# Kernel optimization log

Hardware: AMD Instinct MI355X
Metric: run time of the kernel (lower is better)

The kernel has to match this reference:

```python
import jax, jax.numpy as jnp
import numpy as np

D_MODEL = 1024
HEADS = 16
D_K = D_MODEL // HEADS
B, S = 2, 2048


def setup_inputs() -> dict:
    key = jax.random.key(0)
    ks = jax.random.split(key, 11)
    sc = 1.0 / np.sqrt(D_MODEL)
    return {
        "q": jax.random.normal(ks[0], (B, S, D_MODEL), jnp.float32),
        "k": jax.random.normal(ks[1], (B, S, D_MODEL), jnp.float32),
        "v": jax.random.normal(ks[2], (B, S, D_MODEL), jnp.float32),
        "Wq": jax.random.normal(ks[3], (D_MODEL, D_MODEL), jnp.float32) * sc,
        "bq": jnp.zeros((D_MODEL,), jnp.float32),
        "Wk": jax.random.normal(ks[4], (D_MODEL, D_MODEL), jnp.float32) * sc,
        "bk": jnp.zeros((D_MODEL,), jnp.float32),
        "Wv": jax.random.normal(ks[5], (D_MODEL, D_MODEL), jnp.float32) * sc,
        "bv": jnp.zeros((D_MODEL,), jnp.float32),
        "Wo": jax.random.normal(ks[6], (D_MODEL, D_MODEL), jnp.float32) * sc,
        "bo": jnp.zeros((D_MODEL,), jnp.float32),
    }


def reference(q, k, v, Wq, bq, Wk, bk, Wv, bv, Wo, bo):
    bs = q.shape[0]
    # linear projections then split heads: [B,S,D] -> [B,H,S,Dk]
    def proj(x, W, b):
        y = x @ W.T + b
        return y.reshape(bs, -1, HEADS, D_K).transpose(0, 2, 1, 3)

    qh = proj(q, Wq, bq)
    kh = proj(k, Wk, bk)
    vh = proj(v, Wv, bv)
    # scores: [B,H,Sq,Sk] -- full attention matrix as in the original
    scores = jnp.einsum("bhqd,bhkd->bhqk", qh, kh) / jnp.sqrt(
        jnp.asarray(D_K, jnp.float32))
    attn = jax.nn.softmax(scores, axis=-1)
    # dropout is identity in eval/reference mode
    out = jnp.einsum("bhqk,bhkd->bhqd", attn, vh)
    concat = out.transpose(0, 2, 1, 3).reshape(bs, -1, D_MODEL)
    return concat @ Wo.T + bo
```

## Files before the change

kernel.cpp:

```cpp
#include <hip/hip_runtime.h>
#include <hip/hip_bf16.h>

typedef __attribute__((ext_vector_type(8))) short bf16x8;
typedef __attribute__((ext_vector_type(4))) float f32x4;
typedef __attribute__((ext_vector_type(16))) float f32x16;

#define DM   1024
#define SEQ  2048
#define NB   2
#define NH   16
#define MR   (NB*SEQ)

#define SMK  (MR*DM)
#define W1M  (DM*DM)

#define QSCALE 0.18033688011112042f

#define OFF_QB  ((size_t)0)
#define OFF_WO  ((size_t)(3*(size_t)SMK + 3*(size_t)W1M))
#define OFF_QP  ((size_t)(3*(size_t)SMK + 4*(size_t)W1M))
#define OFF_KP  ((size_t)(4*(size_t)SMK + 4*(size_t)W1M))
#define OFF_VP  ((size_t)(5*(size_t)SMK + 4*(size_t)W1M))
#define OFF_CC  ((size_t)0)

__device__ __forceinline__ unsigned short f2bf(float f) {
  union { __hip_bfloat16 b; unsigned short u; } cv;
  cv.b = __float2bfloat16(f);
  return cv.u;
}

__device__ __forceinline__ unsigned int cvtpk_bf16(float lo, float hi) {
  unsigned int r;
  asm("v_cvt_pk_bf16_f32 %0, %1, %2" : "=v"(r) : "v"(lo), "v"(hi));
  return r;
}

__device__ __forceinline__ void plane32_swap(unsigned int& a, unsigned int& b) {
  asm("v_permlane32_swap_b32 %0, %1" : "+v"(a), "+v"(b));
}

__global__ __launch_bounds__(256) void cvt_wo(const float* __restrict__ wo,
                                              unsigned short* __restrict__ dst) {
  int i = blockIdx.x * 256 + threadIdx.x;
  float4 v = reinterpret_cast<const float4*>(wo)[i];
  ushort4 o;
  o.x = f2bf(v.x); o.y = f2bf(v.y); o.z = f2bf(v.z); o.w = f2bf(v.w);
  reinterpret_cast<ushort4*>(dst)[i] = o;
}

__device__ __forceinline__ void gload_lds16(const void* g, void* l) {
  __builtin_amdgcn_global_load_lds(
      (const __attribute__((address_space(1))) unsigned int*)g,
      (__attribute__((address_space(3))) unsigned int*)l,
      16, 0, 0);
}

template<bool BIAS_ROW>
__device__ __forceinline__ void gemm_f32_body(unsigned short* __restrict__ As,
                                              unsigned short* __restrict__ Bs,
                                              const float* __restrict__ A,
                                              const float* __restrict__ B,
                                              const float* __restrict__ bias,
                                              unsigned short* __restrict__ C,
                                              int N, int K, float scale,
                                              int brow, int bcol) {
  const int tid  = threadIdx.x;
  const int lane = tid & 63;
  const int w    = tid >> 6;
  const int wr   = w >> 1, wc = w & 1;

  f32x4 acc[4][4];
#pragma unroll
  for (int m = 0; m < 4; m++)
#pragma unroll
    for (int n = 0; n < 4; n++) acc[m][n] = (f32x4){0.f, 0.f, 0.f, 0.f};

  const int srow = lane >> 2;
  const int scol = (lane & 3) * 8;

  f32x4 fa[2][2], fb[2][2];

  auto loadst = [&](int k0) {
#pragma unroll
    for (int i = 0; i < 2; i++) {
      const float* pa = A + (size_t)(brow + (w + i * 4) * 16 + srow) * K + k0 + scol;
      fa[i][0] = *(const f32x4*)pa;
      fa[i][1] = *(const f32x4*)(pa + 4);
      const float* pb = B + (size_t)(bcol + (w + i * 4) * 16 + srow) * K + k0 + scol;
      fb[i][0] = *(const f32x4*)pb;
      fb[i][1] = *(const f32x4*)(pb + 4);
    }
  };
  auto commit = [&](int buf) {
#pragma unroll
    for (int i = 0; i < 2; i++) {
      union { unsigned int u[4]; bf16x8 v8; } ua, ub;
#pragma unroll
      for (int j = 0; j < 2; j++) {
        ua.u[2 * j]     = cvtpk_bf16(fa[i][j][0], fa[i][j][1]);
        ua.u[2 * j + 1] = cvtpk_bf16(fa[i][j][2], fa[i][j][3]);
        ub.u[2 * j]     = cvtpk_bf16(fb[i][j][0], fb[i][j][1]);
        ub.u[2 * j + 1] = cvtpk_bf16(fb[i][j][2], fb[i][j][3]);
      }
      *(bf16x8*)((char*)As + (size_t)buf * 8192 + (w + i * 4) * 1024 + lane * 16) = ua.v8;
      *(bf16x8*)((char*)Bs + (size_t)buf * 8192 + (w + i * 4) * 1024 + lane * 16) = ub.v8;
    }
  };

  loadst(0);
  commit(0);
  loadst(32);

  const int nk = K / 32;
  const int lrow_a = wr * 64 + (lane & 15);
  const int lrow_b = wc * 64 + (lane & 15);
  const int lcol   = (lane >> 4) * 8;

  for (int kt = 0; kt < nk; ++kt) {
    int buf = kt & 1;
    asm volatile("s_waitcnt lgkmcnt(0)" ::: "memory");
    __builtin_amdgcn_s_barrier();
    __builtin_amdgcn_sched_barrier(0);
    if (kt + 1 < nk) commit(buf ^ 1);
    if (kt + 2 < nk) loadst((kt + 2) * 32);
    bf16x8 a[4], b[4];
#pragma unroll
    for (int m = 0; m < 4; m++)
      a[m] = *(const bf16x8*)&As[(size_t)buf * 4096 + (lrow_a + m * 16) * 32 + lcol];
#pragma unroll
    for (int n = 0; n < 4; n++)
      b[n] = *(const bf16x8*)&Bs[(size_t)buf * 4096 + (lrow_b + n * 16) * 32 + lcol];
    __builtin_amdgcn_s_setprio(1);
#pragma unroll
    for (int m = 0; m < 4; m++)
#pragma unroll
      for (int n = 0; n < 4; n++)
        acc[m][n] = __builtin_amdgcn_mfma_f32_16x16x32_bf16(a[m], b[n], acc[m][n], 0, 0, 0);
    __builtin_amdgcn_s_setprio(0);
  }

  const int crow0 = brow + wr * 64;
  const int ccol0 = bcol + wc * 64;
  const int rsub  = (lane >> 4) * 4;
  const int csub  = lane & 15;
#pragma unroll
  for (int m = 0; m < 4; m++)
#pragma unroll
    for (int n = 0; n < 4; n++) {
      int col = ccol0 + n * 16 + csub;
      float bcol_v = BIAS_ROW ? 0.f : bias[col];
#pragma unroll
      for (int qq = 0; qq < 4; qq++) {
        int row = crow0 + m * 16 + rsub + qq;
        float bb = BIAS_ROW ? bias[row] : bcol_v;
        C[(size_t)row * N + col] = f2bf((acc[m][n][qq] + bb) * scale);
      }
    }
}

__global__ __launch_bounds__(256, 3) void gemm_qkv(const float* __restrict__ q,
                                                   const float* __restrict__ k,
                                                   const float* __restrict__ v,
                                                   const float* __restrict__ Wq,
                                                   const float* __restrict__ Wk,
                                                   const float* __restrict__ Wv,
                                                   unsigned short* ws,
                                                   const float* __restrict__ bq,
                                                   const float* __restrict__ bk,
                                                   const float* __restrict__ bv) {
  __shared__ unsigned short As[2 * 128 * 32];
  __shared__ unsigned short Bs[2 * 128 * 32];
  const int i  = blockIdx.x;
  const int x  = i & 7;
  const int r  = i >> 3;
  const int pm = r >> 3;
  const int bx = r & 7;
  const int p  = x * 12 + pm;
  const int z  = p >> 5;
  const int by = p & 31;
  if (z < 2) {
    gemm_f32_body<false>(As, Bs,
                         z ? k : q, z ? Wk : Wq, z ? bk : bq,
                         ws + OFF_QP + (size_t)z * SMK,
                         DM, DM, z ? 1.f : QSCALE, by * 128, bx * 128);
  } else {
    gemm_f32_body<true>(As, Bs,
                        Wv, v, bv,
                        ws + OFF_VP,
                        MR, DM, 1.f, bx * 128, by * 128);
  }
}

__device__ __forceinline__ void gemm_out_body(unsigned short* __restrict__ As,
                                              unsigned short* __restrict__ Bs,
                                              const unsigned short* __restrict__ A,
                                              const unsigned short* __restrict__ Bt,
                                              const float* __restrict__ bias,
                                              float* __restrict__ Cv,
                                              int N, int K,
                                              int brow, int bcol) {
  constexpr int BM = 64, BN = 128;
  const int tid  = threadIdx.x;
  const int lane = tid & 63;
  const int w    = tid >> 6;
  const int wr   = w >> 1, wc = w & 1;

  f32x4 acc[2][4];
#pragma unroll
  for (int m = 0; m < 2; m++)
#pragma unroll
    for (int n = 0; n < 4; n++) acc[m][n] = (f32x4){0.f, 0.f, 0.f, 0.f};

  const int srow = lane >> 2;
  const int scol = (lane & 3) * 8;

  auto stage = [&](int buf, int k0) {
#pragma unroll
    for (int c = w; c < BM / 16; c += 4)
      gload_lds16(A + (size_t)(brow + c * 16 + srow) * K + k0 + scol,
                  (char*)As + (size_t)buf * BM * 64 + c * 1024);
#pragma unroll
    for (int c = w; c < BN / 16; c += 4)
      gload_lds16(Bt + (size_t)(bcol + c * 16 + srow) * K + k0 + scol,
                  (char*)Bs + (size_t)buf * BN * 64 + c * 1024);
  };

  stage(0, 0);
  stage(1, 32);

  const int nk = K / 32;
  const int lrow_a = wr * (BM / 2) + (lane & 15);
  const int lrow_b = wc * (BN / 2) + (lane & 15);
  const int lcol   = (lane >> 4) * 8;

  int b0 = 0;
  for (int kt = 0; kt < nk; ++kt) {
    if (kt + 1 < nk) asm volatile("s_waitcnt vmcnt(3)" ::: "memory");
    else             asm volatile("s_waitcnt vmcnt(0)" ::: "memory");
    __builtin_amdgcn_s_barrier();
    __builtin_amdgcn_sched_barrier(0);
    if (kt + 2 < nk) {
      int bn = b0 + 2; if (bn >= 3) bn -= 3;
      stage(bn, (kt + 2) * 32);
    }
    bf16x8 a[2], b[4];
#pragma unroll
    for (int m = 0; m < 2; m++)
      a[m] = *(const bf16x8*)&As[(size_t)b0 * BM * 32 + (lrow_a + m * 16) * 32 + lcol];
#pragma unroll
    for (int n = 0; n < 4; n++)
      b[n] = *(const bf16x8*)&Bs[(size_t)b0 * BN * 32 + (lrow_b + n * 16) * 32 + lcol];
    __builtin_amdgcn_s_setprio(1);
#pragma unroll
    for (int m = 0; m < 2; m++)
#pragma unroll
      for (int n = 0; n < 4; n++)
        acc[m][n] = __builtin_amdgcn_mfma_f32_16x16x32_bf16(a[m], b[n], acc[m][n], 0, 0, 0);
    __builtin_amdgcn_s_setprio(0);
    b0 = (b0 == 2) ? 0 : b0 + 1;
  }

  const int crow0 = brow + wr * (BM / 2);
  const int ccol0 = bcol + wc * (BN / 2);
  const int rsub  = (lane >> 4) * 4;
  const int csub  = lane & 15;
#pragma unroll
  for (int m = 0; m < 2; m++)
#pragma unroll
    for (int n = 0; n < 4; n++) {
      int col = ccol0 + n * 16 + csub;
      float bv = bias[col];
#pragma unroll
      for (int qq = 0; qq < 4; qq++) {
        int row = crow0 + m * 16 + rsub + qq;
        Cv[(size_t)row * N + col] = acc[m][n][qq] + bv;
      }
    }
}

__global__ __launch_bounds__(256) void gemm_out(const unsigned short* __restrict__ ws,
                                                const float* __restrict__ bo,
                                                float* __restrict__ out) {
  __shared__ unsigned short As[3 * 64 * 32];
  __shared__ unsigned short Bs[3 * 128 * 32];
  const int i  = blockIdx.x;
  const int x  = i & 7;
  const int r  = i >> 3;
  const int pm = r >> 3;
  const int bx = r & 7;
  const int by = x * 8 + pm;
  gemm_out_body(As, Bs,
                ws + OFF_CC, ws + OFF_WO, bo, out,
                DM, DM, by * 64, bx * 128);
}

__global__ __launch_bounds__(512, 4) void flash_attn(unsigned short* ws) {
  __shared__ __align__(16) unsigned char smem[65536];

  const int tid  = threadIdx.x;
  const int lane = tid & 63;
  const int w    = tid >> 6;
  const int s    = w >> 2;
  const int wsub = w & 3;
  const int q    = lane & 31;
  const int hi   = lane >> 5;
  const int swq  = q & 7;
  const int bid  = blockIdx.x;
  const int swzb = (bid & 7) * 64 + (bid >> 3);
  const int qblk = swzb & 15;
  const int bh   = swzb >> 4;
  const int b    = bh >> 4, h = bh & 15;

  const unsigned short* Qp = ws + OFF_QP;
  const unsigned short* Kp = ws + OFF_KP;
  const unsigned short* Vp = ws + OFF_VP;
  unsigned short* CC = ws + OFF_CC;

  const unsigned short* Kg = Kp + (size_t)(b * SEQ) * DM + h * 64;
  const unsigned short* Vg = Vp + (size_t)(h * 64) * MR + (size_t)b * SEQ;

  bf16x8 bqf[4];
  {
    const unsigned short* qrow =
        Qp + (size_t)(b * SEQ + qblk * 128 + wsub * 32 + q) * DM + h * 64;
#pragma unroll
    for (int c = 0; c < 4; c++)
      bqf[c] = *(const bf16x8*)(qrow + c * 16 + hi * 8);
  }

  f32x16 o_acc[2];
#pragma unroll
  for (int dt = 0; dt < 2; dt++)
#pragma unroll
    for (int r = 0; r < 16; r++) o_acc[dt][r] = 0.f;
  float l_run = 0.f;

  auto stage = [&](int buf, int t) {
    const unsigned short* Kt = Kg + (size_t)(s * 16 + t) * 64 * DM;
    const unsigned short* Vt = Vg + (s * 16 + t) * 64;
    char* base = (char*)smem + (size_t)(s * 2 + buf) * 16384;
#pragma unroll
    for (int i = 0; i < 2; i++) {
      int slot = wsub * 128 + i * 64 + lane;
      int srow = slot >> 3;
      int gch  = (slot & 7) ^ (srow & 7);
      gload_lds16(Kt + (size_t)srow * DM + gch * 8, base + slot * 16);
      gload_lds16(Vt + (size_t)srow * MR + gch * 8, base + 8192 + slot * 16);
    }
  };

  stage(0, 0);

  for (int t = 0; t < 16; ++t) {
    int buf = t & 1;
    __syncthreads();
    if (t + 1 < 16) stage(buf ^ 1, t + 1);
    const unsigned short* Kb = (const unsigned short*)(smem + (size_t)(s * 2 + buf) * 16384);
    const unsigned short* Vb = Kb + 4096;

    f32x16 st0, st1;
#pragma unroll
    for (int r = 0; r < 16; r++) { st0[r] = 0.f; st1[r] = 0.f; }
    __builtin_amdgcn_s_setprio(1);
#pragma unroll
    for (int c = 0; c < 4; c++) {
      int ch = (((c << 1) | hi) ^ swq) << 3;
      bf16x8 ak0 = *(const bf16x8*)&Kb[q * 64 + ch];
      bf16x8 ak1 = *(const bf16x8*)&Kb[(32 + q) * 64 + ch];
      st0 = __builtin_amdgcn_mfma_f32_32x32x16_bf16(ak0, bqf[c], st0, 0, 0, 0);
      st1 = __builtin_amdgcn_mfma_f32_32x32x16_bf16(ak1, bqf[c], st1, 0, 0, 0);
    }
    __builtin_amdgcn_s_setprio(0);

    unsigned int pk0[8], pk1[8];
    float lt = 0.f;
#pragma unroll
    for (int p = 0; p < 8; p++) {
      float a0 = __builtin_amdgcn_exp2f(st0[2 * p]);
      float a1 = __builtin_amdgcn_exp2f(st0[2 * p + 1]);
      float b0 = __builtin_amdgcn_exp2f(st1[2 * p]);
      float b1 = __builtin_amdgcn_exp2f(st1[2 * p + 1]);
      lt += (a0 + a1) + (b0 + b1);
      pk0[p] = cvtpk_bf16(a0, a1);
      pk1[p] = cvtpk_bf16(b0, b1);
    }
    l_run += lt;

    plane32_swap(pk0[0], pk0[2]); plane32_swap(pk0[1], pk0[3]);
    plane32_swap(pk0[4], pk0[6]); plane32_swap(pk0[5], pk0[7]);
    plane32_swap(pk1[0], pk1[2]); plane32_swap(pk1[1], pk1[3]);
    plane32_swap(pk1[4], pk1[6]); plane32_swap(pk1[5], pk1[7]);

    __builtin_amdgcn_s_setprio(1);
#pragma unroll
    for (int t4 = 0; t4 < 4; t4++) {
      union { unsigned int u[4]; bf16x8 v; } pb;
      const unsigned int* src = (t4 < 2) ? pk0 : pk1;
      pb.u[0] = src[(t4 & 1) * 4 + 0];
      pb.u[1] = src[(t4 & 1) * 4 + 1];
      pb.u[2] = src[(t4 & 1) * 4 + 2];
      pb.u[3] = src[(t4 & 1) * 4 + 3];
      int ch = (((t4 << 1) | hi) ^ swq) << 3;
#pragma unroll
      for (int dt = 0; dt < 2; dt++) {
        bf16x8 av = *(const bf16x8*)&Vb[(dt * 32 + q) * 64 + ch];
        o_acc[dt] = __builtin_amdgcn_mfma_f32_32x32x16_bf16(av, pb.v, o_acc[dt], 0, 0, 0);
      }
    }
    __builtin_amdgcn_s_setprio(0);
  }

  __syncthreads();
  float* scr = (float*)smem;
  float lsum = l_run + __shfl_xor(l_run, 32, 64);
  if (s == 1) {
    int idx = (wsub * 64 + lane) * 33;
#pragma unroll
    for (int dt = 0; dt < 2; dt++)
#pragma unroll
      for (int r = 0; r < 16; r++) scr[idx + dt * 16 + r] = o_acc[dt][r];
    scr[idx + 32] = lsum;
  }
  __syncthreads();
  if (s == 0) {
    int idx = (wsub * 64 + lane) * 33;
#pragma unroll
    for (int dt = 0; dt < 2; dt++)
#pragma unroll
      for (int r = 0; r < 16; r++) o_acc[dt][r] += scr[idx + dt * 16 + r];
    float l = lsum + scr[idx + 32];
    float inv = 1.f / l;

    int qg = b * SEQ + qblk * 128 + wsub * 32 + q;
    unsigned short* crow = CC + (size_t)qg * DM + h * 64;
#pragma unroll
    for (int dt = 0; dt < 2; dt++)
#pragma unroll
      for (int rq = 0; rq < 4; rq++) {
        ushort4 o;
        o.x = f2bf(o_acc[dt][4 * rq + 0] * inv);
        o.y = f2bf(o_acc[dt][4 * rq + 1] * inv);
        o.z = f2bf(o_acc[dt][4 * rq + 2] * inv);
        o.w = f2bf(o_acc[dt][4 * rq + 3] * inv);
        *(ushort4*)&crow[dt * 32 + rq * 8 + hi * 4] = o;
      }
  }
}

extern "C" void kernel_launch(void* const* d_in, const int* in_sizes, int n_in,
                              void* d_out, int out_size, void* d_ws, size_t ws_size,
                              hipStream_t stream) {
  const float* q  = (const float*)d_in[0];
  const float* k  = (const float*)d_in[1];
  const float* v  = (const float*)d_in[2];
  const float* Wq = (const float*)d_in[3];
  const float* bq = (const float*)d_in[4];
  const float* Wk = (const float*)d_in[5];
  const float* bk = (const float*)d_in[6];
  const float* Wv = (const float*)d_in[7];
  const float* bv = (const float*)d_in[8];
  const float* Wo = (const float*)d_in[9];
  const float* bo = (const float*)d_in[10];

  unsigned short* ws = (unsigned short*)d_ws;
  float* out = (float*)d_out;

  cvt_wo<<<dim3((W1M / 4) / 256), dim3(256), 0, stream>>>(Wo, ws + OFF_WO);

  gemm_qkv<<<dim3(768), dim3(256), 0, stream>>>(q, k, v, Wq, Wk, Wv, ws, bq, bk, bv);

  flash_attn<<<dim3(512), dim3(512), 0, stream>>>(ws);

  gemm_out<<<dim3(512), dim3(256), 0, stream>>>(ws, bo, out);
}
```

Measured before the change: 112.1 us.

## Deepen QKV GEMM pipeline to triple LDS buffers and two register stages

The fp32-input QKV projection GEMM moves from double to triple buffering in shared memory and keeps two register stages of global loads in flight, prefetching three k-tiles ahead. Fragment reads from LDS are now issued before the commit of the next tile, so the LDS write overlaps with the MFMA work. Launch bounds drop from 3 to 2 blocks per CU to allow for the extra registers and shared memory. The deeper prefetch is meant to hide global load latency, at the cost of lower occupancy.

```diff
diff --git a/kernel.cpp b/kernel.cpp
--- a/kernel.cpp
+++ b/kernel.cpp
@@ -78,9 +78,9 @@
   const int srow = lane >> 2;
   const int scol = (lane & 3) * 8;
 
-  f32x4 fa[2][2], fb[2][2];
-
-  auto loadst = [&](int k0) {
+  f32x4 fa0[2][2], fb0[2][2], fa1[2][2], fb1[2][2];
+
+  auto loadst = [&](int k0, f32x4 (&fa)[2][2], f32x4 (&fb)[2][2]) {
 #pragma unroll
     for (int i = 0; i < 2; i++) {
       const float* pa = A + (size_t)(brow + (w + i * 4) * 16 + srow) * K + k0 + scol;
@@ -91,7 +91,7 @@
       fb[i][1] = *(const f32x4*)(pb + 4);
     }
   };
-  auto commit = [&](int buf) {
+  auto commit = [&](int buf, f32x4 (&fa)[2][2], f32x4 (&fb)[2][2]) {
 #pragma unroll
     for (int i = 0; i < 2; i++) {
       union { unsigned int u[4]; bf16x8 v8; } ua, ub;
@@ -107,29 +107,32 @@
     }
   };
 
-  loadst(0);
-  commit(0);
-  loadst(32);
-
   const int nk = K / 32;
   const int lrow_a = wr * 64 + (lane & 15);
   const int lrow_b = wc * 64 + (lane & 15);
   const int lcol   = (lane >> 4) * 8;
 
-  for (int kt = 0; kt < nk; ++kt) {
-    int buf = kt & 1;
+  loadst(0, fa0, fb0);
+  commit(0, fa0, fb0);
+  loadst(32, fa1, fb1);
+  loadst(64, fa0, fb0);
+
+  int b_read = 0;
+
+  auto iter = [&](int kt, f32x4 (&fa)[2][2], f32x4 (&fb)[2][2]) {
     asm volatile("s_waitcnt lgkmcnt(0)" ::: "memory");
     __builtin_amdgcn_s_barrier();
     __builtin_amdgcn_sched_barrier(0);
-    if (kt + 1 < nk) commit(buf ^ 1);
-    if (kt + 2 < nk) loadst((kt + 2) * 32);
+    int b_write = b_read + 1; if (b_write == 3) b_write = 0;
     bf16x8 a[4], b[4];
 #pragma unroll
     for (int m = 0; m < 4; m++)
-      a[m] = *(const bf16x8*)&As[(size_t)buf * 4096 + (lrow_a + m * 16) * 32 + lcol];
+      a[m] = *(const bf16x8*)&As[(size_t)b_read * 4096 + (lrow_a + m * 16) * 32 + lcol];
 #pragma unroll
     for (int n = 0; n < 4; n++)
-      b[n] = *(const bf16x8*)&Bs[(size_t)buf * 4096 + (lrow_b + n * 16) * 32 + lcol];
+      b[n] = *(const bf16x8*)&Bs[(size_t)b_read * 4096 + (lrow_b + n * 16) * 32 + lcol];
+    if (kt + 1 < nk) commit(b_write, fa, fb);
+    if (kt + 3 < nk) loadst((kt + 3) * 32, fa, fb);
     __builtin_amdgcn_s_setprio(1);
 #pragma unroll
     for (int m = 0; m < 4; m++)
@@ -137,6 +140,12 @@
       for (int n = 0; n < 4; n++)
         acc[m][n] = __builtin_amdgcn_mfma_f32_16x16x32_bf16(a[m], b[n], acc[m][n], 0, 0, 0);
     __builtin_amdgcn_s_setprio(0);
+    b_read = b_write;
+  };
+
+  for (int kt = 0; kt < nk; kt += 2) {
+    iter(kt,     fa1, fb1);
+    iter(kt + 1, fa0, fb0);
   }
 
   const int crow0 = brow + wr * 64;
@@ -158,7 +167,7 @@
     }
 }
 
-__global__ __launch_bounds__(256, 3) void gemm_qkv(const float* __restrict__ q,
+__global__ __launch_bounds__(256, 2) void gemm_qkv(const float* __restrict__ q,
                                                    const float* __restrict__ k,
                                                    const float* __restrict__ v,
                                                    const float* __restrict__ Wq,
@@ -168,8 +177,8 @@
                                                    const float* __restrict__ bq,
                                                    const float* __restrict__ bk,
                                                    const float* __restrict__ bv) {
-  __shared__ unsigned short As[2 * 128 * 32];
-  __shared__ unsigned short Bs[2 * 128 * 32];
+  __shared__ unsigned short As[3 * 128 * 32];
+  __shared__ unsigned short Bs[3 * 128 * 32];
   const int i  = blockIdx.x;
   const int x  = i & 7;
   const int r  = i >> 3;
```

Measured after the change: 114.3 us. 2.0% more time.

## Pre-convert weights and V to bf16, stream fp32 A via LDS-direct triple buffer

Applied to the files above, without the earlier changes.

Wq, Wk, Wo and the v activations are converted to bf16 in one fused pre-pass, so the QKV GEMM reads bf16 B operands. The fp32 A operand is now loaded straight into LDS with global_load_lds into an XOR-swizzled layout and converted to bf16 at fragment-read time, replacing the register-staged load-convert-store pipeline. Staging moves from a double to a triple buffer with vmcnt-based waits, and occupancy drops from 3 to 2 blocks per SM because of the larger LDS footprint. The extra conversion pass adds one more trip through global memory for v and the weights.

```diff
diff --git a/kernel.cpp b/kernel.cpp
--- a/kernel.cpp
+++ b/kernel.cpp
@@ -17,6 +17,8 @@
 #define QSCALE 0.18033688011112042f
 
 #define OFF_QB  ((size_t)0)
+#define OFF_KB  ((size_t)SMK)
+#define OFF_WQB ((size_t)(3*(size_t)SMK))
 #define OFF_WO  ((size_t)(3*(size_t)SMK + 3*(size_t)W1M))
 #define OFF_QP  ((size_t)(3*(size_t)SMK + 4*(size_t)W1M))
 #define OFF_KP  ((size_t)(4*(size_t)SMK + 4*(size_t)W1M))
@@ -39,13 +41,29 @@
   asm("v_permlane32_swap_b32 %0, %1" : "+v"(a), "+v"(b));
 }
 
-__global__ __launch_bounds__(256) void cvt_wo(const float* __restrict__ wo,
-                                              unsigned short* __restrict__ dst) {
+__global__ __launch_bounds__(256) void cvt_all(const float* __restrict__ wq,
+                                               const float* __restrict__ wk,
+                                               const float* __restrict__ wo,
+                                               const float* __restrict__ v,
+                                               unsigned short* __restrict__ ws) {
   int i = blockIdx.x * 256 + threadIdx.x;
-  float4 v = reinterpret_cast<const float4*>(wo)[i];
+  const float* src;
+  unsigned short* dst;
+  int j;
+  if (i < 3 * (W1M / 4)) {
+    int z = i >> 18;
+    j = i & ((W1M / 4) - 1);
+    src = (z == 0) ? wq : ((z == 1) ? wk : wo);
+    dst = ws + ((z == 2) ? OFF_WO : OFF_WQB + (size_t)z * W1M);
+  } else {
+    j = i - 3 * (W1M / 4);
+    src = v;
+    dst = ws + OFF_KB;
+  }
+  float4 val = reinterpret_cast<const float4*>(src)[j];
   ushort4 o;
-  o.x = f2bf(v.x); o.y = f2bf(v.y); o.z = f2bf(v.z); o.w = f2bf(v.w);
-  reinterpret_cast<ushort4*>(dst)[i] = o;
+  o.x = f2bf(val.x); o.y = f2bf(val.y); o.z = f2bf(val.z); o.w = f2bf(val.w);
+  reinterpret_cast<ushort4*>(dst)[j] = o;
 }
 
 __device__ __forceinline__ void gload_lds16(const void* g, void* l) {
@@ -56,10 +74,10 @@
 }
 
 template<bool BIAS_ROW>
-__device__ __forceinline__ void gemm_f32_body(unsigned short* __restrict__ As,
+__device__ __forceinline__ void gemm_hyb_body(unsigned char* __restrict__ Afs,
                                               unsigned short* __restrict__ Bs,
                                               const float* __restrict__ A,
-                                              const float* __restrict__ B,
+                                              const unsigned short* __restrict__ B,
                                               const float* __restrict__ bias,
                                               unsigned short* __restrict__ C,
                                               int N, int K, float scale,
@@ -75,61 +93,62 @@
 #pragma unroll
     for (int n = 0; n < 4; n++) acc[m][n] = (f32x4){0.f, 0.f, 0.f, 0.f};
 
+  const int arow_l = lane >> 3;
+  const int agch   = (lane & 7) ^ arow_l;
   const int srow = lane >> 2;
   const int scol = (lane & 3) * 8;
 
-  f32x4 fa[2][2], fb[2][2];
-
-  auto loadst = [&](int k0) {
-#pragma unroll
-    for (int i = 0; i < 2; i++) {
-      const float* pa = A + (size_t)(brow + (w + i * 4) * 16 + srow) * K + k0 + scol;
-      fa[i][0] = *(const f32x4*)pa;
-      fa[i][1] = *(const f32x4*)(pa + 4);
-      const float* pb = B + (size_t)(bcol + (w + i * 4) * 16 + srow) * K + k0 + scol;
-      fb[i][0] = *(const f32x4*)pb;
-      fb[i][1] = *(const f32x4*)(pb + 4);
-    }
+  auto stage = [&](int buf, int k0) {
+#pragma unroll
+    for (int ii = 0; ii < 4; ii++) {
+      int j = w * 4 + ii;
+      gload_lds16(A + (size_t)(brow + j * 8 + arow_l) * K + k0 + agch * 4,
+                  Afs + (size_t)buf * 16384 + j * 1024);
+    }
+#pragma unroll
+    for (int c = w; c < 8; c += 4)
+      gload_lds16(B + (size_t)(bcol + c * 16 + srow) * K + k0 + scol,
+                  (char*)Bs + (size_t)buf * 8192 + c * 1024);
   };
-  auto commit = [&](int buf) {
-#pragma unroll
-    for (int i = 0; i < 2; i++) {
-      union { unsigned int u[4]; bf16x8 v8; } ua, ub;
-#pragma unroll
-      for (int j = 0; j < 2; j++) {
-        ua.u[2 * j]     = cvtpk_bf16(fa[i][j][0], fa[i][j][1]);
-        ua.u[2 * j + 1] = cvtpk_bf16(fa[i][j][2], fa[i][j][3]);
-        ub.u[2 * j]     = cvtpk_bf16(fb[i][j][0], fb[i][j][1]);
-        ub.u[2 * j + 1] = cvtpk_bf16(fb[i][j][2], fb[i][j][3]);
-      }
-      *(bf16x8*)((char*)As + (size_t)buf * 8192 + (w + i * 4) * 1024 + lane * 16) = ua.v8;
-      *(bf16x8*)((char*)Bs + (size_t)buf * 8192 + (w + i * 4) * 1024 + lane * 16) = ub.v8;
-    }
-  };
-
-  loadst(0);
-  commit(0);
-  loadst(32);
+
+  stage(0, 0);
+  stage(1, 32);
 
   const int nk = K / 32;
+  const int g      = lane >> 4;
   const int lrow_a = wr * 64 + (lane & 15);
   const int lrow_b = wc * 64 + (lane & 15);
-  const int lcol   = (lane >> 4) * 8;
-
+  const int lcol   = g * 8;
+  const int s0 = (2 * g) ^ (lane & 7);
+  const int s1 = (2 * g + 1) ^ (lane & 7);
+
+  int b0 = 0;
   for (int kt = 0; kt < nk; ++kt) {
-    int buf = kt & 1;
-    asm volatile("s_waitcnt lgkmcnt(0)" ::: "memory");
+    if (kt + 1 < nk) asm volatile("s_waitcnt vmcnt(6)" ::: "memory");
+    else             asm volatile("s_waitcnt vmcnt(0)" ::: "memory");
     __builtin_amdgcn_s_barrier();
     __builtin_amdgcn_sched_barrier(0);
-    if (kt + 1 < nk) commit(buf ^ 1);
-    if (kt + 2 < nk) loadst((kt + 2) * 32);
+    if (kt + 2 < nk) {
+      int bn = b0 + 2; if (bn >= 3) bn -= 3;
+      stage(bn, (kt + 2) * 32);
+    }
+    const unsigned char* Ab = Afs + (size_t)b0 * 16384;
     bf16x8 a[4], b[4];
 #pragma unroll
-    for (int m = 0; m < 4; m++)
-      a[m] = *(const bf16x8*)&As[(size_t)buf * 4096 + (lrow_a + m * 16) * 32 + lcol];
+    for (int m = 0; m < 4; m++) {
+      int R = lrow_a + m * 16;
+      f32x4 lo = *(const f32x4*)(Ab + R * 128 + s0 * 16);
+      f32x4 hi = *(const f32x4*)(Ab + R * 128 + s1 * 16);
+      union { unsigned int u[4]; bf16x8 v8; } ua;
+      ua.u[0] = cvtpk_bf16(lo[0], lo[1]);
+      ua.u[1] = cvtpk_bf16(lo[2], lo[3]);
+      ua.u[2] = cvtpk_bf16(hi[0], hi[1]);
+      ua.u[3] = cvtpk_bf16(hi[2], hi[3]);
+      a[m] = ua.v8;
+    }
 #pragma unroll
     for (int n = 0; n < 4; n++)
-      b[n] = *(const bf16x8*)&Bs[(size_t)buf * 4096 + (lrow_b + n * 16) * 32 + lcol];
+      b[n] = *(const bf16x8*)&Bs[(size_t)b0 * 4096 + (lrow_b + n * 16) * 32 + lcol];
     __builtin_amdgcn_s_setprio(1);
 #pragma unroll
     for (int m = 0; m < 4; m++)
@@ -137,6 +156,7 @@
       for (int n = 0; n < 4; n++)
         acc[m][n] = __builtin_amdgcn_mfma_f32_16x16x32_bf16(a[m], b[n], acc[m][n], 0, 0, 0);
     __builtin_amdgcn_s_setprio(0);
+    b0 = (b0 == 2) ? 0 : b0 + 1;
   }
 
   const int crow0 = brow + wr * 64;
@@ -158,18 +178,15 @@
     }
 }
 
-__global__ __launch_bounds__(256, 3) void gemm_qkv(const float* __restrict__ q,
+__global__ __launch_bounds__(256, 2) void gemm_qkv(const float* __restrict__ q,
                                                    const float* __restrict__ k,
-                                                   const float* __restrict__ v,
-                                                   const float* __restrict__ Wq,
-                                                   const float* __restrict__ Wk,
                                                    const float* __restrict__ Wv,
                                                    unsigned short* ws,
                                                    const float* __restrict__ bq,
                                                    const float* __restrict__ bk,
                                                    const float* __restrict__ bv) {
-  __shared__ unsigned short As[2 * 128 * 32];
-  __shared__ unsigned short Bs[2 * 128 * 32];
+  __shared__ __align__(16) unsigned char Afs[3 * 16384];
+  __shared__ unsigned short Bs[3 * 4096];
   const int i  = blockIdx.x;
   const int x  = i & 7;
   const int r  = i >> 3;
@@ -179,13 +196,13 @@
   const int z  = p >> 5;
   const int by = p & 31;
   if (z < 2) {
-    gemm_f32_body<false>(As, Bs,
-                         z ? k : q, z ? Wk : Wq, z ? bk : bq,
+    gemm_hyb_body<false>(Afs, Bs,
+                         z ? k : q, ws + OFF_WQB + (size_t)z * W1M, z ? bk : bq,
                          ws + OFF_QP + (size_t)z * SMK,
                          DM, DM, z ? 1.f : QSCALE, by * 128, bx * 128);
   } else {
-    gemm_f32_body<true>(As, Bs,
-                        Wv, v, bv,
+    gemm_hyb_body<true>(Afs, Bs,
+                        Wv, ws + OFF_KB, bv,
                         ws + OFF_VP,
                         MR, DM, 1.f, bx * 128, by * 128);
   }
@@ -465,9 +482,10 @@
   unsigned short* ws = (unsigned short*)d_ws;
   float* out = (float*)d_out;
 
-  cvt_wo<<<dim3((W1M / 4) / 256), dim3(256), 0, stream>>>(Wo, ws + OFF_WO);
-
-  gemm_qkv<<<dim3(768), dim3(256), 0, stream>>>(q, k, v, Wq, Wk, Wv, ws, bq, bk, bv);
+  cvt_all<<<dim3((3 * (W1M / 4) + SMK / 4) / 256), dim3(256), 0, stream>>>(
+      Wq, Wk, Wo, v, ws);
+
+  gemm_qkv<<<dim3(768), dim3(256), 0, stream>>>(q, k, Wv, ws, bq, bk, bv);
 
   flash_attn<<<dim3(512), dim3(512), 0, stream>>>(ws);
 
```

Measured after the change: 130.1 us. 1.16x slower.
